# Kernel tuning notes

Measured on AMD Instinct MI355X. Metric: run time of the kernel, lower is better.

Reference implementation:

```python
import jax, jax.numpy as jnp
import numpy as np

B, S, D, H, DH, G, C, FF = 4, 4096, 768, 12, 64, 64, 256, 3072


def _ln(x, g, b):
    m = x.mean(-1, keepdims=True)
    v = ((x - m) ** 2).mean(-1, keepdims=True)
    return (x - m) * jax.lax.rsqrt(v + 1e-5) * g + b


def setup_inputs() -> dict:
    key = jax.random.key(0)
    ks = jax.random.split(key, 20)
    w = lambda k, shape: jax.random.normal(k, shape, jnp.float32) * 0.02
    inp = dict(
        cur_input=jax.random.normal(ks[0], (B, S, D), jnp.float32),
        prevLayerOutput=jax.random.normal(ks[1], (B, S, D), jnp.float32),
        classVector=jax.random.normal(ks[2], (B, C), jnp.float32),
        rand_idx=jax.random.randint(ks[3], (B, G), 0, S),
        # self-attention (rand+global) projections
        Wq=w(ks[4], (D, D)), bq=jnp.zeros(D), Wk=w(ks[5], (D, D)), bk=jnp.zeros(D),
        Wv=w(ks[6], (D, D)), bv=jnp.zeros(D), Wo=w(ks[7], (D, D)), bo=jnp.zeros(D),
        g1=jnp.ones(D), b1=jnp.zeros(D),
        # cross-attention over class vector (k/v feature dim is 1 after unsqueeze(-1))
        Wqc=w(ks[8], (D, D)), bqc=jnp.zeros(D), Wkc=w(ks[9], (1, D)), bkc=jnp.zeros(D),
        Wvc=w(ks[10], (1, D)), bvc=jnp.zeros(D), Woc=w(ks[11], (D, D)), boc=jnp.zeros(D),
        g2=jnp.ones(D), b2=jnp.zeros(D),
        # feed-forward
        W1=w(ks[12], (D, FF)), bf1=jnp.zeros(FF), W2=w(ks[13], (FF, D)), bf2=jnp.zeros(D),
        g3=jnp.ones(D), b3=jnp.zeros(D),
    )
    return inp


def reference(cur_input, prevLayerOutput, classVector, rand_idx,
              Wq, bq, Wk, bk, Wv, bv, Wo, bo, g1, b1,
              Wqc, bqc, Wkc, bkc, Wvc, bvc, Woc, boc, g2, b2,
              W1, bf1, W2, bf2, g3, b3):
    scale = np.float32(1.0 / np.sqrt(DH))
    # ---- masked multi-head self attention over global + random tokens ----
    q = (cur_input @ Wq + bq).reshape(B, S, H, DH)
    k = (prevLayerOutput @ Wk + bk).reshape(B, S, H, DH)
    v = (prevLayerOutput @ Wv + bv).reshape(B, S, H, DH)
    sel = jnp.concatenate([jnp.broadcast_to(jnp.arange(G), (B, G)), rand_idx], axis=1)  # [B,2G]
    idx = jnp.broadcast_to(sel[:, :, None, None], (B, 2 * G, H, DH))
    ksel = jnp.take_along_axis(k, idx, axis=1)  # [B,2G,H,DH]
    vsel = jnp.take_along_axis(v, idx, axis=1)
    scores = jnp.einsum('bshd,bkhd->bhsk', q, ksel) * scale  # [B,H,S,2G]
    mask = sel[:, None, None, :] <= jnp.arange(S)[None, None, :, None]  # causal wrt key position
    scores = jnp.where(mask, scores, jnp.float32(-1e9))
    attn = jax.nn.softmax(scores, axis=-1)
    o = jnp.einsum('bhsk,bkhd->bshd', attn, vsel).reshape(B, S, D) @ Wo + bo
    x1 = _ln(cur_input + o, g1, b1)
    # ---- cross attention over class vector (kv seq = C, kv feat = 1) ----
    cv = classVector[:, :, None]  # [B,C,1]
    qc = (x1 @ Wqc + bqc).reshape(B, S, H, DH)
    kc = (cv @ Wkc + bkc).reshape(B, C, H, DH)
    vc = (cv @ Wvc + bvc).reshape(B, C, H, DH)
    sc = jnp.einsum('bshd,bchd->bhsc', qc, kc) * scale
    ac = jax.nn.softmax(sc, axis=-1)
    oc = jnp.einsum('bhsc,bchd->bshd', ac, vc).reshape(B, S, D) @ Woc + boc
    x2 = _ln(x1 + oc, g2, b2)
    # ---- feed forward ----
    ff = jax.nn.relu(x2 @ W1 + bf1) @ W2 + bf2
    return _ln(x2 + ff, g3, b3)
```

## Files before the change

### kernel.cpp

```cpp
#include <hip/hip_runtime.h>
#include <hip/hip_bf16.h>

#define B_ 4
#define S_ 4096
#define D_ 768
#define H_ 12
#define DH_ 64
#define G_ 64
#define C_ 256
#define FF_ 3072

typedef __attribute__((ext_vector_type(8))) short bf16x8;
typedef __attribute__((ext_vector_type(4))) float f32x4;
typedef unsigned short u16;

__device__ __forceinline__ float bfu2f(u16 u) {
    return __uint_as_float((unsigned)u << 16);
}

__device__ __forceinline__ void gload16(const __hip_bfloat16* g, __hip_bfloat16* l) {
    __builtin_amdgcn_global_load_lds(
        (__attribute__((address_space(1))) void*)(void*)const_cast<__hip_bfloat16*>(g),
        (__attribute__((address_space(3))) void*)(void*)l,
        16, 0, 0);
}

__global__ __launch_bounds__(256) void gemm_mfma(
    const __hip_bfloat16* __restrict__ A, const __hip_bfloat16* __restrict__ Bt,
    const float* __restrict__ bias, float* __restrict__ Cf,
    __hip_bfloat16* __restrict__ Cb,
    int M, int N, int K, int lda, int ldbt, int flags)
{
    __shared__ __hip_bfloat16 As[2][128 * 32];
    __shared__ __hip_bfloat16 Bs[2][128 * 32];

    const int t = threadIdx.x;
    const int lane = t & 63;
    const int wave = t >> 6;
    const int wr = wave >> 1, wc = wave & 1;
    const int qd = lane >> 4, r = lane & 15;

    int lin = blockIdx.y * gridDim.x + blockIdx.x;
    int nwg = gridDim.x * gridDim.y;
    int cpx = nwg >> 3;
    int swz = (lin & 7) * cpx + (lin >> 3);
    int bm = (swz / gridDim.x) * 128;
    int bn = (swz % gridDim.x) * 128;

    const int srow = lane >> 2;
    const int scol = (lane & 3) * 8;
    const __hip_bfloat16* gA0 = A + (size_t)(bm + wave * 32 + srow) * lda + scol;
    const __hip_bfloat16* gA1 = gA0 + (size_t)16 * lda;
    const __hip_bfloat16* gB0 = Bt + (size_t)(bn + wave * 32 + srow) * ldbt + scol;
    const __hip_bfloat16* gB1 = gB0 + (size_t)16 * ldbt;

    f32x4 acc[4][4] = {};

    gload16(gA0, &As[0][wave * 1024]);
    gload16(gA1, &As[0][wave * 1024 + 512]);
    gload16(gB0, &Bs[0][wave * 1024]);
    gload16(gB1, &Bs[0][wave * 1024 + 512]);
    __syncthreads();

    int cur = 0;
    for (int k0 = 0; k0 < K; k0 += 32, cur ^= 1) {
        if (k0 + 32 < K) {
            int kn = k0 + 32, nb = cur ^ 1;
            gload16(gA0 + kn, &As[nb][wave * 1024]);
            gload16(gA1 + kn, &As[nb][wave * 1024 + 512]);
            gload16(gB0 + kn, &Bs[nb][wave * 1024]);
            gload16(gB1 + kn, &Bs[nb][wave * 1024 + 512]);
        }
        bf16x8 afr[4], bfr[4];
#pragma unroll
        for (int m = 0; m < 4; ++m)
            afr[m] = *(const bf16x8*)&As[cur][(wr * 64 + m * 16 + r) * 32 + qd * 8];
#pragma unroll
        for (int n = 0; n < 4; ++n)
            bfr[n] = *(const bf16x8*)&Bs[cur][(wc * 64 + n * 16 + r) * 32 + qd * 8];
#pragma unroll
        for (int m = 0; m < 4; ++m)
#pragma unroll
            for (int n = 0; n < 4; ++n)
                acc[m][n] = __builtin_amdgcn_mfma_f32_16x16x32_bf16(
                    afr[m], bfr[n], acc[m][n], 0, 0, 0);
        __syncthreads();
    }

#pragma unroll
    for (int m = 0; m < 4; ++m) {
        int row0 = bm + wr * 64 + m * 16 + qd * 4;
#pragma unroll
        for (int n = 0; n < 4; ++n) {
            int col = bn + wc * 64 + n * 16 + r;
            float bv = (flags & 1) ? bias[col] : 0.0f;
#pragma unroll
            for (int i = 0; i < 4; ++i) {
                float v = acc[m][n][i] + bv;
                if (flags & 2) v = fmaxf(v, 0.0f);
                size_t off = (size_t)(row0 + i) * N + col;
                if (flags & 4) v += Cf[off];
                if (flags & 8) Cb[off] = __float2bfloat16(v);
                else           Cf[off] = v;
            }
        }
    }
}

__global__ __launch_bounds__(256) void conv_bf16(const float* __restrict__ in,
                                                 __hip_bfloat16* __restrict__ out,
                                                 int n8)
{
    int i = blockIdx.x * 256 + threadIdx.x;
    if (i >= n8) return;
    const float4* p = (const float4*)(in + (size_t)i * 8);
    float4 v0 = p[0], v1 = p[1];
    __hip_bfloat16 o[8] = {
        __float2bfloat16(v0.x), __float2bfloat16(v0.y),
        __float2bfloat16(v0.z), __float2bfloat16(v0.w),
        __float2bfloat16(v1.x), __float2bfloat16(v1.y),
        __float2bfloat16(v1.z), __float2bfloat16(v1.w)};
    *(uint4*)(out + (size_t)i * 8) = *(const uint4*)o;
}

__global__ __launch_bounds__(256) void transp_all(
    const float* __restrict__ Wq, const float* __restrict__ Wo,
    const float* __restrict__ Wk, const float* __restrict__ Wv,
    const float* __restrict__ W1, const float* __restrict__ W2,
    __hip_bfloat16* __restrict__ Wqt, __hip_bfloat16* __restrict__ Wot,
    __hip_bfloat16* __restrict__ Wkt, __hip_bfloat16* __restrict__ Wvt,
    __hip_bfloat16* __restrict__ W1t, __hip_bfloat16* __restrict__ W2t)
{
    int tile = blockIdx.x;
    const float* W; __hip_bfloat16* Wt; int K, N;
    if (tile < 2304) {
        int w = tile / 576; tile -= w * 576;
        K = 768; N = 768;
        W  = (w == 0) ? Wq : (w == 1) ? Wo : (w == 2) ? Wk : Wv;
        Wt = (w == 0) ? Wqt : (w == 1) ? Wot : (w == 2) ? Wkt : Wvt;
    } else if (tile < 4608) { tile -= 2304; K = 768; N = 3072; W = W1; Wt = W1t; }
    else                    { tile -= 4608; K = 3072; N = 768; W = W2; Wt = W2t; }
    int ntx = N >> 5;
    int k0 = (tile / ntx) * 32, n0 = (tile % ntx) * 32;
    __shared__ float s[32][33];
    int tx = threadIdx.x & 31, ty = threadIdx.x >> 5;
#pragma unroll
    for (int i = 0; i < 4; ++i)
        s[ty + i * 8][tx] = W[(size_t)(k0 + ty + i * 8) * N + n0 + tx];
    __syncthreads();
#pragma unroll
    for (int i = 0; i < 4; ++i)
        Wt[(size_t)(n0 + ty + i * 8) * K + k0 + tx] =
            __float2bfloat16(s[tx][ty + i * 8]);
}

__global__ void gather_kernel(const float* __restrict__ prev,
                              const int* __restrict__ rand_idx,
                              __hip_bfloat16* __restrict__ Pselb,
                              int* __restrict__ sel)
{
    int j = blockIdx.x;
    int b = j >> 7, i = j & 127;
    int sv = (i < 64) ? i : rand_idx[b * G_ + (i - 64)];
    if (threadIdx.x == 0) sel[j] = sv;
    const float* src = prev + ((size_t)(b * S_ + sv)) * D_;
    __hip_bfloat16* dst = Pselb + (size_t)j * D_;
    for (int d = threadIdx.x; d < D_; d += blockDim.x)
        dst[d] = __float2bfloat16(src[d]);
}

__global__ __launch_bounds__(256) void attn3_kernel(
    const u16* __restrict__ qb, const u16* __restrict__ kb,
    const u16* __restrict__ vb, const int* __restrict__ sel,
    u16* __restrict__ out)
{
    const int bh = blockIdx.y;
    const int b = bh / H_, h = bh % H_;
    const int s0 = blockIdx.x * 256;
    const int t = threadIdx.x;
    const int w = t >> 6, lane = t & 63;
    const int r = lane & 15, qd = lane >> 4;

    __shared__ u16 Vt[64][136];
    __shared__ u16 Plds[4][32][136];
    __shared__ int ssel[128];

    {
        int key0 = t >> 4;
        int d0 = (t & 15) * 4;
        for (int kk = key0; kk < 128; kk += 16) {
            ushort4 v = *(const ushort4*)(vb + (size_t)(b * 128 + kk) * D_ + h * 64 + d0);
            Vt[d0 + 0][kk] = v.x; Vt[d0 + 1][kk] = v.y;
            Vt[d0 + 2][kk] = v.z; Vt[d0 + 3][kk] = v.w;
        }
        if (t < 128) ssel[t] = sel[b * 128 + t];
    }
    __syncthreads();

    int selv[8];
#pragma unroll
    for (int n = 0; n < 8; ++n) selv[n] = ssel[n * 16 + r];

    for (int pass = 0; pass < 2; ++pass) {
        const int sbase = s0 + w * 64 + pass * 32;
        f32x4 accs[2][8] = {};

#pragma unroll
        for (int ks = 0; ks < 2; ++ks) {
            bf16x8 af[2];
#pragma unroll
            for (int m = 0; m < 2; ++m)
                af[m] = *(const bf16x8*)(qb + (size_t)(b * S_ + sbase + m * 16 + r) * D_ + h * 64 + ks * 32 + qd * 8);
#pragma unroll
            for (int n = 0; n < 8; ++n) {
                bf16x8 bfv = *(const bf16x8*)(kb + (size_t)(b * 128 + n * 16 + r) * D_ + h * 64 + ks * 32 + qd * 8);
#pragma unroll
                for (int m = 0; m < 2; ++m)
                    accs[m][n] = __builtin_amdgcn_mfma_f32_16x16x32_bf16(
                        af[m], bfv, accs[m][n], 0, 0, 0);
            }
        }

#pragma unroll
        for (int m = 0; m < 2; ++m) {
#pragma unroll
            for (int i = 0; i < 4; ++i) {
                int srow = sbase + m * 16 + qd * 4 + i;
                float pm = -3e38f;
#pragma unroll
                for (int n = 0; n < 8; ++n) {
                    float sc = accs[m][n][i] * 0.125f;
                    if (selv[n] > srow) sc = -1e9f;
                    accs[m][n][i] = sc;
                    pm = fmaxf(pm, sc);
                }
#pragma unroll
                for (int off = 1; off < 16; off <<= 1)
                    pm = fmaxf(pm, __shfl_xor(pm, off, 64));
                float ps = 0.f;
#pragma unroll
                for (int n = 0; n < 8; ++n) {
                    float e = __expf(accs[m][n][i] - pm);
                    accs[m][n][i] = e;
                    ps += e;
                }
#pragma unroll
                for (int off = 1; off < 16; off <<= 1)
                    ps += __shfl_xor(ps, off, 64);
                float inv = 1.0f / ps;
#pragma unroll
                for (int n = 0; n < 8; ++n)
                    accs[m][n][i] *= inv;
            }
        }

#pragma unroll
        for (int m = 0; m < 2; ++m)
#pragma unroll
            for (int n = 0; n < 8; ++n)
#pragma unroll
                for (int i = 0; i < 4; ++i) {
                    __hip_bfloat16 pb = __float2bfloat16(accs[m][n][i]);
                    Plds[w][m * 16 + qd * 4 + i][n * 16 + r] = *(u16*)&pb;
                }

        f32x4 acco[2][4] = {};
#pragma unroll
        for (int ks = 0; ks < 4; ++ks) {
            bf16x8 pa[2];
#pragma unroll
            for (int m = 0; m < 2; ++m)
                pa[m] = *(const bf16x8*)&Plds[w][m * 16 + r][ks * 32 + qd * 8];
#pragma unroll
            for (int nd = 0; nd < 4; ++nd) {
                bf16x8 bv = *(const bf16x8*)&Vt[nd * 16 + r][ks * 32 + qd * 8];
#pragma unroll
                for (int m = 0; m < 2; ++m)
                    acco[m][nd] = __builtin_amdgcn_mfma_f32_16x16x32_bf16(
                        pa[m], bv, acco[m][nd], 0, 0, 0);
            }
        }

#pragma unroll
        for (int m = 0; m < 2; ++m)
#pragma unroll
            for (int nd = 0; nd < 4; ++nd)
#pragma unroll
                for (int i = 0; i < 4; ++i) {
                    __hip_bfloat16 ob = __float2bfloat16(acco[m][nd][i]);
                    out[(size_t)(b * S_ + sbase + m * 16 + qd * 4 + i) * D_ + h * 64 + nd * 16 + r] = *(u16*)&ob;
                }
    }
}

__global__ __launch_bounds__(192) void addln_bb(
    const u16* __restrict__ xa, const u16* __restrict__ xb,
    const float* __restrict__ g, const float* __restrict__ beta,
    float* __restrict__ out)
{
    const int row = blockIdx.x;
    const int t = threadIdx.x;
    const ushort4 a = ((const ushort4*)(xa + (size_t)row * D_))[t];
    const ushort4 b4 = ((const ushort4*)(xb + (size_t)row * D_))[t];
    float v[4] = {bfu2f(a.x) + bfu2f(b4.x), bfu2f(a.y) + bfu2f(b4.y),
                  bfu2f(a.z) + bfu2f(b4.z), bfu2f(a.w) + bfu2f(b4.w)};
    float sum = v[0] + v[1] + v[2] + v[3];
#pragma unroll
    for (int off = 1; off < 64; off <<= 1) sum += __shfl_xor(sum, off, 64);
    __shared__ float r1[3], r2[3];
    int wv = t >> 6, ln = t & 63;
    if (ln == 0) r1[wv] = sum;
    __syncthreads();
    float mean = (r1[0] + r1[1] + r1[2]) * (1.0f / 768.0f);
    float sq = 0.f;
#pragma unroll
    for (int i = 0; i < 4; ++i) { v[i] -= mean; sq += v[i] * v[i]; }
#pragma unroll
    for (int off = 1; off < 64; off <<= 1) sq += __shfl_xor(sq, off, 64);
    if (ln == 0) r2[wv] = sq;
    __syncthreads();
    float var = (r2[0] + r2[1] + r2[2]) * (1.0f / 768.0f);
    float rs = rsqrtf(var + 1e-5f);
    float4 gg = ((const float4*)g)[t];
    float4 bb = ((const float4*)beta)[t];
    float4 o;
    o.x = v[0] * rs * gg.x + bb.x;
    o.y = v[1] * rs * gg.y + bb.y;
    o.z = v[2] * rs * gg.z + bb.z;
    o.w = v[3] * rs * gg.w + bb.w;
    ((float4*)(out + (size_t)row * D_))[t] = o;
}

__global__ __launch_bounds__(256) void precompute_U(
    const float* __restrict__ Wqc, const float* __restrict__ Wkc,
    const float* __restrict__ bqc, float* __restrict__ Ut, float* __restrict__ ab)
{
    __shared__ __attribute__((aligned(16))) float wk[D_];
    for (int i = threadIdx.x; i < D_; i += 256) wk[i] = Wkc[i];
    __syncthreads();
    int idx = blockIdx.x * 256 + threadIdx.x;
    int h = idx / D_, d = idx - h * D_;
    const float4* row = (const float4*)(Wqc + (size_t)d * D_ + h * 64);
    const float4* wkv = (const float4*)(wk + h * 64);
    float a0 = 0.f, a1 = 0.f, a2 = 0.f, a3 = 0.f;
#pragma unroll
    for (int j = 0; j < 16; j += 4) {
        float4 r0 = row[j], r1 = row[j + 1], r2 = row[j + 2], r3 = row[j + 3];
        float4 c0 = wkv[j], c1 = wkv[j + 1], c2 = wkv[j + 2], c3 = wkv[j + 3];
        a0 += r0.x * c0.x + r0.y * c0.y + r0.z * c0.z + r0.w * c0.w;
        a1 += r1.x * c1.x + r1.y * c1.y + r1.z * c1.z + r1.w * c1.w;
        a2 += r2.x * c2.x + r2.y * c2.y + r2.z * c2.z + r2.w * c2.w;
        a3 += r3.x * c3.x + r3.y * c3.y + r3.z * c3.z + r3.w * c3.w;
    }
    Ut[idx] = (a0 + a1) + (a2 + a3);
    if (idx < H_) {
        const float4* bq4 = (const float4*)(bqc + idx * 64);
        const float4* wk4 = (const float4*)(wk + idx * 64);
        float s = 0.f;
#pragma unroll
        for (int j = 0; j < 16; ++j) {
            float4 bb = bq4[j], cc = wk4[j];
            s += bb.x * cc.x + bb.y * cc.y + bb.z * cc.z + bb.w * cc.w;
        }
        ab[idx] = s;
    }
}

__global__ __launch_bounds__(256) void precompute_mix(
    const float* __restrict__ Wvc, const float* __restrict__ Woc,
    float* __restrict__ Wmix)
{
    __shared__ float wv[D_];
    for (int i = threadIdx.x; i < D_; i += 256) wv[i] = Wvc[i];
    __syncthreads();
    int idx = blockIdx.x * 256 + threadIdx.x;
    int h = idx / D_, n = idx - h * D_;
    float acc[8] = {};
#pragma unroll
    for (int j = 0; j < 64; ++j)
        acc[j & 7] += wv[h * 64 + j] * Woc[(size_t)(h * 64 + j) * D_ + n];
    Wmix[idx] = ((acc[0] + acc[1]) + (acc[2] + acc[3]))
              + ((acc[4] + acc[5]) + (acc[6] + acc[7]));
}

__global__ __launch_bounds__(256) void precompute_bias2(
    const float* __restrict__ Woc, const float* __restrict__ bvc,
    const float* __restrict__ boc, float* __restrict__ bias2)
{
    int tx = threadIdx.x & 63, ty = threadIdx.x >> 6;
    int n = blockIdx.x * 64 + tx;
    int d0 = ty * 192;
    float a = 0.f;
#pragma unroll 8
    for (int d = 0; d < 192; ++d)
        a += bvc[d0 + d] * Woc[(size_t)(d0 + d) * D_ + n];
    __shared__ float red[4][64];
    red[ty][tx] = a;
    __syncthreads();
    if (ty == 0)
        bias2[n] = boc[n] + red[0][tx] + red[1][tx] + red[2][tx] + red[3][tx];
}

__global__ __launch_bounds__(256) void fused_mid(
    const float* __restrict__ cur, const u16* __restrict__ oprojb,
    const float* __restrict__ g1, const float* __restrict__ b1,
    const float* __restrict__ Ut, const float* __restrict__ ab,
    const float* __restrict__ cvec,
    const float* __restrict__ Wmix, const float* __restrict__ bias2,
    const float* __restrict__ g2, const float* __restrict__ b2,
    __hip_bfloat16* __restrict__ x2b)
{
    const int w = threadIdx.x >> 6, lane = threadIdx.x & 63;
    const int row0 = blockIdx.x * 8 + w * 2;
    const int b = blockIdx.x >> 9;

    __shared__ float4 cvs[64];
    __shared__ float xp[4][64][28];
    __shared__ float muls[4][24];

    if (threadIdx.x < 64)
        cvs[threadIdx.x] = ((const float4*)(cvec + b * C_))[threadIdx.x];

    float4 x1[2][3];
#pragma unroll
    for (int rr = 0; rr < 2; ++rr) {
        const float4* pa = (const float4*)(cur + (size_t)(row0 + rr) * D_);
        const ushort4* pb = (const ushort4*)(oprojb + (size_t)(row0 + rr) * D_);
        float s = 0.f;
#pragma unroll
        for (int i = 0; i < 3; ++i) {
            float4 a = pa[i * 64 + lane];
            ushort4 ou = pb[i * 64 + lane];
            float4 v;
            v.x = a.x + bfu2f(ou.x); v.y = a.y + bfu2f(ou.y);
            v.z = a.z + bfu2f(ou.z); v.w = a.w + bfu2f(ou.w);
            x1[rr][i] = v;
            s += v.x + v.y + v.z + v.w;
        }
#pragma unroll
        for (int off = 1; off < 64; off <<= 1) s += __shfl_xor(s, off, 64);
        float mean = s * (1.0f / 768.0f);
        float sq = 0.f;
#pragma unroll
        for (int i = 0; i < 3; ++i) {
            x1[rr][i].x -= mean; x1[rr][i].y -= mean;
            x1[rr][i].z -= mean; x1[rr][i].w -= mean;
            sq += x1[rr][i].x * x1[rr][i].x + x1[rr][i].y * x1[rr][i].y
                + x1[rr][i].z * x1[rr][i].z + x1[rr][i].w * x1[rr][i].w;
        }
#pragma unroll
        for (int off = 1; off < 64; off <<= 1) sq += __shfl_xor(sq, off, 64);
        float rs = rsqrtf(sq * (1.0f / 768.0f) + 1e-5f);
#pragma unroll
        for (int i = 0; i < 3; ++i) {
            float4 gg = ((const float4*)g1)[i * 64 + lane];
            float4 bb = ((const float4*)b1)[i * 64 + lane];
            x1[rr][i].x = x1[rr][i].x * rs * gg.x + bb.x;
            x1[rr][i].y = x1[rr][i].y * rs * gg.y + bb.y;
            x1[rr][i].z = x1[rr][i].z * rs * gg.z + bb.z;
            x1[rr][i].w = x1[rr][i].w * rs * gg.w + bb.w;
        }
    }

    float acc[24];
#pragma unroll
    for (int j = 0; j < 24; ++j) acc[j] = 0.f;
#pragma unroll
    for (int i = 0; i < 3; ++i) {
#pragma unroll
        for (int h = 0; h < 12; ++h) {
            float4 u = ((const float4*)(Ut + (size_t)h * D_))[i * 64 + lane];
#pragma unroll
            for (int rr = 0; rr < 2; ++rr)
                acc[rr * 12 + h] += x1[rr][i].x * u.x + x1[rr][i].y * u.y
                                  + x1[rr][i].z * u.z + x1[rr][i].w * u.w;
        }
    }
#pragma unroll
    for (int j4 = 0; j4 < 6; ++j4)
        *(float4*)&xp[w][lane][j4 * 4] = *(float4*)&acc[j4 * 4];
    __syncthreads();

    if (lane < 48) {
        int j = lane >> 1, half = lane & 1;
        float ssum = 0.f;
#pragma unroll
        for (int k = 0; k < 32; ++k) ssum += xp[w][half * 32 + k][j];
        ssum += __shfl_xor(ssum, 1, 64);
        float a = 0.125f * (ssum + ab[j % 12]);
        float z = 0.f, ms = 0.f;
#pragma unroll
        for (int it = 0; it < 32; ++it) {
            float4 c = cvs[half * 32 + it];
            float e0 = __expf(a * c.x), e1 = __expf(a * c.y),
                  e2 = __expf(a * c.z), e3 = __expf(a * c.w);
            z += e0 + e1 + e2 + e3;
            ms += e0 * c.x + e1 * c.y + e2 * c.z + e3 * c.w;
        }
        z += __shfl_xor(z, 1, 64);
        ms += __shfl_xor(ms, 1, 64);
        if (half == 0) muls[w][j] = ms / z;
    }
    __syncthreads();

    float4 t2[2][3];
#pragma unroll
    for (int i = 0; i < 3; ++i) {
        float4 bv = ((const float4*)bias2)[i * 64 + lane];
        float4 o0 = bv, o1 = bv;
#pragma unroll
        for (int h = 0; h < 12; ++h) {
            float4 wm = ((const float4*)(Wmix + (size_t)h * D_))[i * 64 + lane];
            float m0 = muls[w][h], m1 = muls[w][12 + h];
            o0.x += m0 * wm.x; o0.y += m0 * wm.y; o0.z += m0 * wm.z; o0.w += m0 * wm.w;
            o1.x += m1 * wm.x; o1.y += m1 * wm.y; o1.z += m1 * wm.z; o1.w += m1 * wm.w;
        }
        t2[0][i].x = x1[0][i].x + o0.x; t2[0][i].y = x1[0][i].y + o0.y;
        t2[0][i].z = x1[0][i].z + o0.z; t2[0][i].w = x1[0][i].w + o0.w;
        t2[1][i].x = x1[1][i].x + o1.x; t2[1][i].y = x1[1][i].y + o1.y;
        t2[1][i].z = x1[1][i].z + o1.z; t2[1][i].w = x1[1][i].w + o1.w;
    }

#pragma unroll
    for (int rr = 0; rr < 2; ++rr) {
        float s = 0.f;
#pragma unroll
        for (int i = 0; i < 3; ++i)
            s += t2[rr][i].x + t2[rr][i].y + t2[rr][i].z + t2[rr][i].w;
#pragma unroll
        for (int off = 1; off < 64; off <<= 1) s += __shfl_xor(s, off, 64);
        float mean = s * (1.0f / 768.0f);
        float sq = 0.f;
#pragma unroll
        for (int i = 0; i < 3; ++i) {
            t2[rr][i].x -= mean; t2[rr][i].y -= mean;
            t2[rr][i].z -= mean; t2[rr][i].w -= mean;
            sq += t2[rr][i].x * t2[rr][i].x + t2[rr][i].y * t2[rr][i].y
                + t2[rr][i].z * t2[rr][i].z + t2[rr][i].w * t2[rr][i].w;
        }
#pragma unroll
        for (int off = 1; off < 64; off <<= 1) sq += __shfl_xor(sq, off, 64);
        float rs = rsqrtf(sq * (1.0f / 768.0f) + 1e-5f);
        size_t base = (size_t)(row0 + rr) * D_;
#pragma unroll
        for (int i = 0; i < 3; ++i) {
            float4 gg = ((const float4*)g2)[i * 64 + lane];
            float4 bb = ((const float4*)b2)[i * 64 + lane];
            float vx = t2[rr][i].x * rs * gg.x + bb.x;
            float vy = t2[rr][i].y * rs * gg.y + bb.y;
            float vz = t2[rr][i].z * rs * gg.z + bb.z;
            float vw = t2[rr][i].w * rs * gg.w + bb.w;
            __hip_bfloat16 pk[4] = {
                __float2bfloat16(vx), __float2bfloat16(vy),
                __float2bfloat16(vz), __float2bfloat16(vw)};
            *(uint2*)(x2b + base + i * 256 + lane * 4) = *(const uint2*)pk;
        }
    }
}

extern "C" void kernel_launch(void* const* d_in, const int* in_sizes, int n_in,
                              void* d_out, int out_size, void* d_ws, size_t ws_size,
                              hipStream_t stream) {
    const float* cur   = (const float*)d_in[0];
    const float* prev  = (const float*)d_in[1];
    const float* cvec  = (const float*)d_in[2];
    const int*   ridx  = (const int*)d_in[3];
    const float* Wq  = (const float*)d_in[4];
    const float* bq  = (const float*)d_in[5];
    const float* Wk  = (const float*)d_in[6];
    const float* bk  = (const float*)d_in[7];
    const float* Wv  = (const float*)d_in[8];
    const float* bv  = (const float*)d_in[9];
    const float* Wo  = (const float*)d_in[10];
    const float* bo  = (const float*)d_in[11];
    const float* g1  = (const float*)d_in[12];
    const float* b1  = (const float*)d_in[13];
    const float* Wqc = (const float*)d_in[14];
    const float* bqc = (const float*)d_in[15];
    const float* Wkc = (const float*)d_in[16];
    const float* bkc = (const float*)d_in[17];  (void)bkc;
    const float* Wvc = (const float*)d_in[18];
    const float* bvc = (const float*)d_in[19];
    const float* Woc = (const float*)d_in[20];
    const float* boc = (const float*)d_in[21];
    const float* g2  = (const float*)d_in[22];
    const float* b2  = (const float*)d_in[23];
    const float* W1  = (const float*)d_in[24];
    const float* bf1 = (const float*)d_in[25];
    const float* W2  = (const float*)d_in[26];
    const float* bf2 = (const float*)d_in[27];
    const float* g3  = (const float*)d_in[28];
    const float* b3  = (const float*)d_in[29];
    float* outp = (float*)d_out;
    (void)ws_size; (void)in_sizes; (void)n_in; (void)out_size;

    const int M = B_ * S_;
    const size_t NBSD = (size_t)M * D_;
    const size_t NSEL = (size_t)B_ * 128 * D_;

    __hip_bfloat16* hidb  = (__hip_bfloat16*)d_ws;
    __hip_bfloat16* bf0   = hidb + (size_t)M * FF_;
    __hip_bfloat16* tmpb  = bf0 + NBSD;
    __hip_bfloat16* Pselb = tmpb + NBSD;
    __hip_bfloat16* kselb = Pselb + NSEL;
    __hip_bfloat16* vselb = kselb + NSEL;
    __hip_bfloat16* Wqt   = vselb + NSEL;
    __hip_bfloat16* Wot   = Wqt + (size_t)D_ * D_;
    __hip_bfloat16* Wkt   = Wot + (size_t)D_ * D_;
    __hip_bfloat16* Wvt   = Wkt + (size_t)D_ * D_;
    __hip_bfloat16* W1t   = Wvt + (size_t)D_ * D_;
    __hip_bfloat16* W2t   = W1t + (size_t)D_ * FF_;
    float* Ub    = (float*)(W2t + (size_t)FF_ * D_);
    float* abv   = Ub + (size_t)D_ * H_;
    float* Wmix  = abv + 16;
    float* bias2 = Wmix + (size_t)H_ * D_;
    int*   selb  = (int*)(bias2 + D_);

    gather_kernel<<<B_ * 128, 256, 0, stream>>>(prev, ridx, Pselb, selb);
    transp_all<<<6912, 256, 0, stream>>>(Wq, Wo, Wk, Wv, W1, W2,
                                         Wqt, Wot, Wkt, Wvt, W1t, W2t);
    conv_bf16<<<(int)(NBSD / 8 + 255) / 256, 256, 0, stream>>>(cur, bf0, (int)(NBSD / 8));
    precompute_U<<<36, 256, 0, stream>>>(Wqc, Wkc, bqc, Ub, abv);
    precompute_mix<<<36, 256, 0, stream>>>(Wvc, Woc, Wmix);
    precompute_bias2<<<12, 256, 0, stream>>>(Woc, bvc, boc, bias2);

    {
        dim3 g(D_ / 128, (B_ * 128) / 128);
        gemm_mfma<<<g, 256, 0, stream>>>(Pselb, Wkt, bk, nullptr, kselb,
                                         B_ * 128, D_, D_, D_, D_, 1 | 8);
        gemm_mfma<<<g, 256, 0, stream>>>(Pselb, Wvt, bv, nullptr, vselb,
                                         B_ * 128, D_, D_, D_, D_, 1 | 8);
    }

    gemm_mfma<<<dim3(D_ / 128, M / 128), 256, 0, stream>>>(
        bf0, Wqt, bq, nullptr, tmpb, M, D_, D_, D_, D_, 1 | 8);

    attn3_kernel<<<dim3(S_ / 256, B_ * H_), 256, 0, stream>>>(
        (const u16*)tmpb, (const u16*)kselb, (const u16*)vselb, selb, (u16*)bf0);

    gemm_mfma<<<dim3(D_ / 128, M / 128), 256, 0, stream>>>(
        bf0, Wot, bo, nullptr, tmpb, M, D_, D_, D_, D_, 1 | 8);

    fused_mid<<<M / 8, 256, 0, stream>>>(
        cur, (const u16*)tmpb, g1, b1, Ub, abv, cvec, Wmix, bias2, g2, b2, bf0);

    gemm_mfma<<<dim3(FF_ / 128, M / 128), 256, 0, stream>>>(
        bf0, W1t, bf1, nullptr, hidb, M, FF_, D_, D_, D_, 1 | 2 | 8);
    gemm_mfma<<<dim3(D_ / 128, M / 128), 256, 0, stream>>>(
        hidb, W2t, bf2, nullptr, tmpb, M, D_, FF_, FF_, FF_, 1 | 8);

    addln_bb<<<M, 192, 0, stream>>>((const u16*)bf0, (const u16*)tmpb, g3, b3, outp);
}
```

Measured before the change: 465.5 us.

## Add 256x256-tile 512-thread MFMA GEMM and use it for the big projections

```diff
diff --git a/kernel.cpp b/kernel.cpp
--- a/kernel.cpp
+++ b/kernel.cpp
@@ -23,6 +23,105 @@
         (__attribute__((address_space(1))) void*)(void*)const_cast<__hip_bfloat16*>(g),
         (__attribute__((address_space(3))) void*)(void*)l,
         16, 0, 0);
+}
+
+__global__ __launch_bounds__(512) void gemm256(
+    const u16* __restrict__ A, const u16* __restrict__ Bt,
+    const float* __restrict__ bias, u16* __restrict__ Cb,
+    int M, int N, int K, int flags)
+{
+    __shared__ __attribute__((aligned(16))) u16 As[2][256 * 64];
+    __shared__ __attribute__((aligned(16))) u16 Bs[2][256 * 64];
+
+    const int tid = threadIdx.x;
+    const int lane = tid & 63, w = tid >> 6;
+    const int wm = w >> 2, wn = w & 3;
+    const int r = lane & 15, qd = lane >> 4;
+
+    int lin = blockIdx.y * gridDim.x + blockIdx.x;
+    int nwg = gridDim.x * gridDim.y;
+    int cpx = nwg >> 3;
+    int swz = (lin & 7) * cpx + (lin >> 3);
+    int bm = (swz / gridDim.x) * 256;
+    int bn = (swz % gridDim.x) * 256;
+
+    const int srow = w * 8 + (lane >> 3);
+    const int scol = ((lane & 7) ^ (lane >> 3)) * 8;
+    const int sdst = w * 512;
+
+#define STAGE256(c, k0)                                                        \
+    {                                                                          \
+        _Pragma("unroll")                                                      \
+        for (int l = 0; l < 4; ++l)                                            \
+            gload16((const __hip_bfloat16*)(A + (size_t)(bm + srow + l * 64) * K + (k0) + scol), \
+                    (__hip_bfloat16*)&As[c][l * 4096 + sdst]);                 \
+        _Pragma("unroll")                                                      \
+        for (int l = 0; l < 4; ++l)                                            \
+            gload16((const __hip_bfloat16*)(Bt + (size_t)(bn + srow + l * 64) * K + (k0) + scol), \
+                    (__hip_bfloat16*)&Bs[c][l * 4096 + sdst]);                 \
+    }
+
+    f32x4 acc[8][4] = {};
+    const int NT = K >> 6;
+
+    STAGE256(0, 0)
+    STAGE256(1, 64)
+    asm volatile("s_waitcnt vmcnt(8)" ::: "memory");
+    __builtin_amdgcn_s_barrier();
+
+    for (int kt = 0; kt < NT; ++kt) {
+        const int c = kt & 1;
+        const u16* as = As[c];
+        const u16* bs = Bs[c];
+#pragma unroll
+        for (int kk = 0; kk < 2; ++kk) {
+            bf16x8 af[8], bfv[4];
+#pragma unroll
+            for (int m = 0; m < 8; ++m) {
+                int row = wm * 128 + m * 16 + r;
+                af[m] = *(const bf16x8*)&as[row * 64 + (((kk << 2) + qd) ^ (r & 7)) * 8];
+            }
+#pragma unroll
+            for (int n = 0; n < 4; ++n) {
+                int row = wn * 64 + n * 16 + r;
+                bfv[n] = *(const bf16x8*)&bs[row * 64 + (((kk << 2) + qd) ^ (r & 7)) * 8];
+            }
+            __builtin_amdgcn_s_setprio(1);
+#pragma unroll
+            for (int m = 0; m < 8; ++m)
+#pragma unroll
+                for (int n = 0; n < 4; ++n)
+                    acc[m][n] = __builtin_amdgcn_mfma_f32_16x16x32_bf16(
+                        af[m], bfv[n], acc[m][n], 0, 0, 0);
+            __builtin_amdgcn_s_setprio(0);
+        }
+        asm volatile("s_waitcnt lgkmcnt(0)" ::: "memory");
+        __builtin_amdgcn_s_barrier();
+        if (kt + 2 < NT) STAGE256(c, (kt + 2) << 6)
+        if (kt + 1 < NT) {
+            if (kt + 2 < NT) asm volatile("s_waitcnt vmcnt(8)" ::: "memory");
+            else             asm volatile("s_waitcnt vmcnt(0)" ::: "memory");
+            __builtin_amdgcn_s_barrier();
+        }
+    }
+
+#pragma unroll
+    for (int m = 0; m < 8; ++m) {
+        int row0 = bm + wm * 128 + m * 16 + qd * 4;
+#pragma unroll
+        for (int n = 0; n < 4; ++n) {
+            int col = bn + wn * 64 + n * 16 + r;
+            float bv = (flags & 1) ? bias[col] : 0.0f;
+#pragma unroll
+            for (int i = 0; i < 4; ++i) {
+                float v = acc[m][n][i] + bv;
+                if (flags & 2) v = fmaxf(v, 0.0f);
+                __hip_bfloat16 ob = __float2bfloat16(v);
+                Cb[(size_t)(row0 + i) * N + col] = *(u16*)&ob;
+            }
+        }
+    }
+#undef STAGE256
 }
 
 __global__ __launch_bounds__(256) void gemm_mfma(
@@ -632,22 +731,22 @@
                                          B_ * 128, D_, D_, D_, D_, 1 | 8);
     }
 
-    gemm_mfma<<<dim3(D_ / 128, M / 128), 256, 0, stream>>>(
-        bf0, Wqt, bq, nullptr, tmpb, M, D_, D_, D_, D_, 1 | 8);
+    gemm256<<<dim3(D_ / 256, M / 256), 512, 0, stream>>>(
+        (const u16*)bf0, (const u16*)Wqt, bq, (u16*)tmpb, M, D_, D_, 1);
 
     attn3_kernel<<<dim3(S_ / 256, B_ * H_), 256, 0, stream>>>(
         (const u16*)tmpb, (const u16*)kselb, (const u16*)vselb, selb, (u16*)bf0);
 
-    gemm_mfma<<<dim3(D_ / 128, M / 128), 256, 0, stream>>>(
-        bf0, Wot, bo, nullptr, tmpb, M, D_, D_, D_, D_, 1 | 8);
+    gemm256<<<dim3(D_ / 256, M / 256), 512, 0, stream>>>(
+        (const u16*)bf0, (const u16*)Wot, bo, (u16*)tmpb, M, D_, D_, 1);
 
     fused_mid<<<M / 8, 256, 0, stream>>>(
         cur, (const u16*)tmpb, g1, b1, Ub, abv, cvec, Wmix, bias2, g2, b2, bf0);
 
-    gemm_mfma<<<dim3(FF_ / 128, M / 128), 256, 0, stream>>>(
-        bf0, W1t, bf1, nullptr, hidb, M, FF_, D_, D_, D_, 1 | 2 | 8);
-    gemm_mfma<<<dim3(D_ / 128, M / 128), 256, 0, stream>>>(
-        hidb, W2t, bf2, nullptr, tmpb, M, D_, FF_, FF_, FF_, 1 | 8);
+    gemm256<<<dim3(FF_ / 256, M / 256), 512, 0, stream>>>(
+        (const u16*)bf0, (const u16*)W1t, bf1, (u16*)hidb, M, FF_, D_, 1 | 2);
+    gemm256<<<dim3(D_ / 256, M / 256), 512, 0, stream>>>(
+        (const u16*)hidb, (const u16*)W2t, bf2, (u16*)tmpb, M, D_, FF_, 1);
 
     addln_bb<<<M, 192, 0, stream>>>((const u16*)bf0, (const u16*)tmpb, g3, b3, outp);
 }
```

After: 450.6 us. 1.03x faster.

## Add 256x256-tile 8-wave pipelined MFMA GEMM for the large projections

Applied to the files above, without the earlier changes.

```diff
diff --git a/kernel.cpp b/kernel.cpp
--- a/kernel.cpp
+++ b/kernel.cpp
@@ -23,6 +23,149 @@
         (__attribute__((address_space(1))) void*)(void*)const_cast<__hip_bfloat16*>(g),
         (__attribute__((address_space(3))) void*)(void*)l,
         16, 0, 0);
+}
+
+__global__ __launch_bounds__(512, 2) void gemm256(
+    const u16* __restrict__ A, const u16* __restrict__ Bt,
+    const float* __restrict__ bias, u16* __restrict__ Cb,
+    int M, int N, int K, int flags)
+{
+    __shared__ __attribute__((aligned(16))) u16 Ah[2][2][128 * 64];
+    __shared__ __attribute__((aligned(16))) u16 Bh[2][2][128 * 64];
+
+    const int tid = threadIdx.x;
+    const int lane = tid & 63, w = tid >> 6;
+    const int wm = w >> 2, wn = w & 3;
+    const int r = lane & 15, qd = lane >> 4;
+
+    int lin = blockIdx.y * gridDim.x + blockIdx.x;
+    int nwg = gridDim.x * gridDim.y;
+    int cpx = nwg >> 3;
+    int swz = (lin & 7) * cpx + (lin >> 3);
+    int bm = (swz / gridDim.x) * 256;
+    int bn = (swz % gridDim.x) * 256;
+
+    const int srow = tid >> 3;
+    const int scol = ((tid & 7) ^ (srow & 7)) * 8;
+    const int sdst = tid * 8;
+
+#define STG_A(c, h, kt) { \
+    const u16* s_ = A + (size_t)(bm + (h) * 128 + srow) * K + ((kt) << 6) + scol; \
+    gload16((const __hip_bfloat16*)s_, (__hip_bfloat16*)&Ah[c][h][sdst]); \
+    gload16((const __hip_bfloat16*)(s_ + (size_t)64 * K), (__hip_bfloat16*)&Ah[c][h][sdst + 4096]); }
+#define STG_B(c, h, kt) { \
+    const u16* s_ = Bt + (size_t)(bn + (h) * 128 + srow) * K + ((kt) << 6) + scol; \
+    gload16((const __hip_bfloat16*)s_, (__hip_bfloat16*)&Bh[c][h][sdst]); \
+    gload16((const __hip_bfloat16*)(s_ + (size_t)64 * K), (__hip_bfloat16*)&Bh[c][h][sdst + 4096]); }
+
+#define GRAN(kk) (((((kk) << 2) + qd) ^ (r & 7)) * 8)
+#define READS_AF(c, mb) { \
+    _Pragma("unroll") for (int m = 0; m < 4; ++m) { \
+        const u16* p_ = &Ah[c][wm][((mb + m) * 16 + r) * 64]; \
+        af[m][0] = *(const bf16x8*)(p_ + GRAN(0)); \
+        af[m][1] = *(const bf16x8*)(p_ + GRAN(1)); } }
+#define READS_BF(dst, c, nb) { \
+    _Pragma("unroll") for (int n = 0; n < 2; ++n) { \
+        const u16* p_ = &Bh[c][wn >> 1][((wn & 1) * 64 + (nb + n) * 16 + r) * 64]; \
+        dst[n][0] = *(const bf16x8*)(p_ + GRAN(0)); \
+        dst[n][1] = *(const bf16x8*)(p_ + GRAN(1)); } }
+#define QMFMA(mb, nb, bfx) { \
+    __builtin_amdgcn_s_setprio(1); \
+    _Pragma("unroll") for (int kk = 0; kk < 2; ++kk) \
+    _Pragma("unroll") for (int m = 0; m < 4; ++m) \
+    _Pragma("unroll") for (int n = 0; n < 2; ++n) \
+        acc[mb + m][nb + n] = __builtin_amdgcn_mfma_f32_16x16x32_bf16( \
+            af[m][kk], bfx[n][kk], acc[mb + m][nb + n], 0, 0, 0); \
+    __builtin_amdgcn_s_setprio(0); }
+#define BAR() __builtin_amdgcn_s_barrier()
+#define LGKM0() asm volatile("s_waitcnt lgkmcnt(0)" ::: "memory")
+
+    f32x4 acc[8][4] = {};
+    const int NT = K >> 6;
+    const int J = NT >> 1;
+
+    STG_A(0, 0, 0) STG_A(0, 1, 0) STG_B(0, 0, 0) STG_B(0, 1, 0)
+    STG_B(1, 0, 1) STG_B(1, 1, 1)
+    asm volatile("s_waitcnt vmcnt(4)" ::: "memory");
+    BAR();
+
+    bf16x8 af[4][2], bf0[2][2], bf1[2][2];
+
+    for (int j = 0; j < J; ++j) {
+        const int to1 = 2 * j + 1;
+        const int te2 = 2 * j + 2;
+        const int to3 = 2 * j + 3;
+        const bool pf = (j < J - 1);
+
+        READS_AF(0, 0) READS_BF(bf0, 0, 0)
+        STG_A(1, 0, to1)
+        BAR(); LGKM0();
+        QMFMA(0, 0, bf0)
+        BAR();
+        READS_BF(bf1, 0, 2)
+        STG_A(1, 1, to1)
+        BAR(); LGKM0();
+        QMFMA(0, 2, bf1)
+        BAR();
+        READS_AF(0, 4)
+        if (pf) { STG_B(0, 0, te2) }
+        BAR(); LGKM0();
+        QMFMA(4, 2, bf1)
+        BAR();
+        if (pf) { STG_B(0, 1, te2) }
+        BAR();
+        QMFMA(4, 0, bf0)
+        if (pf) asm volatile("s_waitcnt vmcnt(4)" ::: "memory");
+        else    asm volatile("s_waitcnt vmcnt(0)" ::: "memory");
+        BAR();
+        READS_AF(1, 0) READS_BF(bf0, 1, 0)
+        if (pf) { STG_A(0, 0, te2) }
+        BAR(); LGKM0();
+        QMFMA(0, 0, bf0)
+        BAR();
+        READS_BF(bf1, 1, 2)
+        if (pf) { STG_A(0, 1, te2) }
+        BAR(); LGKM0();
+        QMFMA(0, 2, bf1)
+        BAR();
+        READS_AF(1, 4)
+        if (pf) { STG_B(1, 0, to3) }
+        BAR(); LGKM0();
+        QMFMA(4, 2, bf1)
+        BAR();
+        if (pf) { STG_B(1, 1, to3) }
+        BAR();
+        QMFMA(4, 0, bf0)
+        if (pf) {
+            asm volatile("s_waitcnt vmcnt(4)" ::: "memory");
+            BAR();
+        }
+    }
+
+#pragma unroll
+    for (int m = 0; m < 8; ++m) {
+        int row0 = bm + wm * 128 + m * 16 + qd * 4;
+#pragma unroll
+        for (int n = 0; n < 4; ++n) {
+            int col = bn + wn * 64 + n * 16 + r;
+            float bv = (flags & 1) ? bias[col] : 0.0f;
+#pragma unroll
+            for (int i = 0; i < 4; ++i) {
+                float v = acc[m][n][i] + bv;
+                if (flags & 2) v = fmaxf(v, 0.0f);
+                __hip_bfloat16 ob = __float2bfloat16(v);
+                Cb[(size_t)(row0 + i) * N + col] = *(u16*)&ob;
+            }
+        }
+    }
+#undef STG_A
+#undef STG_B
+#undef GRAN
+#undef READS_AF
+#undef READS_BF
+#undef QMFMA
+#undef BAR
+#undef LGKM0
 }
 
 __global__ __launch_bounds__(256) void gemm_mfma(
@@ -632,22 +775,22 @@
                                          B_ * 128, D_, D_, D_, D_, 1 | 8);
     }
 
-    gemm_mfma<<<dim3(D_ / 128, M / 128), 256, 0, stream>>>(
-        bf0, Wqt, bq, nullptr, tmpb, M, D_, D_, D_, D_, 1 | 8);
+    gemm256<<<dim3(D_ / 256, M / 256), 512, 0, stream>>>(
+        (const u16*)bf0, (const u16*)Wqt, bq, (u16*)tmpb, M, D_, D_, 1);
 
     attn3_kernel<<<dim3(S_ / 256, B_ * H_), 256, 0, stream>>>(
         (const u16*)tmpb, (const u16*)kselb, (const u16*)vselb, selb, (u16*)bf0);
 
-    gemm_mfma<<<dim3(D_ / 128, M / 128), 256, 0, stream>>>(
-        bf0, Wot, bo, nullptr, tmpb, M, D_, D_, D_, D_, 1 | 8);
+    gemm256<<<dim3(D_ / 256, M / 256), 512, 0, stream>>>(
+        (const u16*)bf0, (const u16*)Wot, bo, (u16*)tmpb, M, D_, D_, 1);
 
     fused_mid<<<M / 8, 256, 0, stream>>>(
         cur, (const u16*)tmpb, g1, b1, Ub, abv, cvec, Wmix, bias2, g2, b2, bf0);
 
-    gemm_mfma<<<dim3(FF_ / 128, M / 128), 256, 0, stream>>>(
-        bf0, W1t, bf1, nullptr, hidb, M, FF_, D_, D_, D_, 1 | 2 | 8);
-    gemm_mfma<<<dim3(D_ / 128, M / 128), 256, 0, stream>>>(
-        hidb, W2t, bf2, nullptr, tmpb, M, D_, FF_, FF_, FF_, 1 | 8);
+    gemm256<<<dim3(FF_ / 256, M / 256), 512, 0, stream>>>(
+        (const u16*)bf0, (const u16*)W1t, bf1, (u16*)hidb, M, FF_, D_, 1 | 2);
+    gemm256<<<dim3(D_ / 256, M / 256), 512, 0, stream>>>(
+        (const u16*)hidb, (const u16*)W2t, bf2, (u16*)tmpb, M, D_, FF_, 1);
 
     addln_bb<<<M, 192, 0, stream>>>((const u16*)bf0, (const u16*)tmpb, g3, b3, outp);
 }
```

Measured after the change: 438.3 us. 5.8% less time.

## Rewrite GEMM as 512-thread BK=64 swizzled-LDS kernel and read bf16 residual

Applied to the files above, without the earlier changes.

```diff
diff --git a/kernel.cpp b/kernel.cpp
--- a/kernel.cpp
+++ b/kernel.cpp
@@ -25,20 +25,18 @@
         16, 0, 0);
 }
 
-__global__ __launch_bounds__(256) void gemm_mfma(
-    const __hip_bfloat16* __restrict__ A, const __hip_bfloat16* __restrict__ Bt,
-    const float* __restrict__ bias, float* __restrict__ Cf,
-    __hip_bfloat16* __restrict__ Cb,
-    int M, int N, int K, int lda, int ldbt, int flags)
-{
-    __shared__ __hip_bfloat16 As[2][128 * 32];
-    __shared__ __hip_bfloat16 Bs[2][128 * 32];
-
-    const int t = threadIdx.x;
-    const int lane = t & 63;
-    const int wave = t >> 6;
-    const int wr = wave >> 1, wc = wave & 1;
-    const int qd = lane >> 4, r = lane & 15;
+__global__ __launch_bounds__(512, 4) void gemm128(
+    const u16* __restrict__ A, const u16* __restrict__ Bt,
+    const float* __restrict__ bias, u16* __restrict__ Cb,
+    int M, int N, int K, int flags)
+{
+    __shared__ __attribute__((aligned(16))) u16 As[2][128 * 64];
+    __shared__ __attribute__((aligned(16))) u16 Bs[2][128 * 64];
+
+    const int tid = threadIdx.x;
+    const int lane = tid & 63, w = tid >> 6;
+    const int wm = w >> 2, wn = w & 3;
+    const int r = lane & 15, qd = lane >> 4;
 
     int lin = blockIdx.y * gridDim.x + blockIdx.x;
     int nwg = gridDim.x * gridDim.y;
@@ -47,64 +45,76 @@
     int bm = (swz / gridDim.x) * 128;
     int bn = (swz % gridDim.x) * 128;
 
-    const int srow = lane >> 2;
-    const int scol = (lane & 3) * 8;
-    const __hip_bfloat16* gA0 = A + (size_t)(bm + wave * 32 + srow) * lda + scol;
-    const __hip_bfloat16* gA1 = gA0 + (size_t)16 * lda;
-    const __hip_bfloat16* gB0 = Bt + (size_t)(bn + wave * 32 + srow) * ldbt + scol;
-    const __hip_bfloat16* gB1 = gB0 + (size_t)16 * ldbt;
-
-    f32x4 acc[4][4] = {};
-
-    gload16(gA0, &As[0][wave * 1024]);
-    gload16(gA1, &As[0][wave * 1024 + 512]);
-    gload16(gB0, &Bs[0][wave * 1024]);
-    gload16(gB1, &Bs[0][wave * 1024 + 512]);
-    __syncthreads();
-
-    int cur = 0;
-    for (int k0 = 0; k0 < K; k0 += 32, cur ^= 1) {
-        if (k0 + 32 < K) {
-            int kn = k0 + 32, nb = cur ^ 1;
-            gload16(gA0 + kn, &As[nb][wave * 1024]);
-            gload16(gA1 + kn, &As[nb][wave * 1024 + 512]);
-            gload16(gB0 + kn, &Bs[nb][wave * 1024]);
-            gload16(gB1 + kn, &Bs[nb][wave * 1024 + 512]);
-        }
-        bf16x8 afr[4], bfr[4];
-#pragma unroll
-        for (int m = 0; m < 4; ++m)
-            afr[m] = *(const bf16x8*)&As[cur][(wr * 64 + m * 16 + r) * 32 + qd * 8];
-#pragma unroll
-        for (int n = 0; n < 4; ++n)
-            bfr[n] = *(const bf16x8*)&Bs[cur][(wc * 64 + n * 16 + r) * 32 + qd * 8];
-#pragma unroll
-        for (int m = 0; m < 4; ++m)
-#pragma unroll
-            for (int n = 0; n < 4; ++n)
-                acc[m][n] = __builtin_amdgcn_mfma_f32_16x16x32_bf16(
-                    afr[m], bfr[n], acc[m][n], 0, 0, 0);
-        __syncthreads();
+    const int srow = tid >> 3;
+    const int sg = ((tid & 7) ^ (srow & 7)) * 8;
+
+#define STG(c, kt) { \
+    const u16* a_ = A + (size_t)(bm + srow) * K + ((kt) << 6) + sg; \
+    gload16((const __hip_bfloat16*)a_, (__hip_bfloat16*)&As[c][tid * 8]); \
+    gload16((const __hip_bfloat16*)(a_ + (size_t)64 * K), (__hip_bfloat16*)&As[c][4096 + tid * 8]); \
+    const u16* b_ = Bt + (size_t)(bn + srow) * K + ((kt) << 6) + sg; \
+    gload16((const __hip_bfloat16*)b_, (__hip_bfloat16*)&Bs[c][tid * 8]); \
+    gload16((const __hip_bfloat16*)(b_ + (size_t)64 * K), (__hip_bfloat16*)&Bs[c][4096 + tid * 8]); }
+
+#define GR(kk) (((((kk) << 2) + qd) ^ (r & 7)) * 8)
+
+    f32x4 acc[4][2] = {};
+    const int NT = K >> 6;
+
+    STG(0, 0)
+    STG(1, 1)
+    asm volatile("s_waitcnt vmcnt(4)" ::: "memory");
+    __builtin_amdgcn_s_barrier();
+
+    for (int kt = 0; kt < NT; ++kt) {
+        const int c = kt & 1;
+        const u16* as = As[c];
+        const u16* bs = Bs[c];
+#pragma unroll
+        for (int kk = 0; kk < 2; ++kk) {
+            bf16x8 af[4], bf[2];
+#pragma unroll
+            for (int m = 0; m < 4; ++m)
+                af[m] = *(const bf16x8*)&as[(wm * 64 + m * 16 + r) * 64 + GR(kk)];
+#pragma unroll
+            for (int n = 0; n < 2; ++n)
+                bf[n] = *(const bf16x8*)&bs[(wn * 32 + n * 16 + r) * 64 + GR(kk)];
+            __builtin_amdgcn_s_setprio(1);
+#pragma unroll
+            for (int m = 0; m < 4; ++m)
+#pragma unroll
+                for (int n = 0; n < 2; ++n)
+                    acc[m][n] = __builtin_amdgcn_mfma_f32_16x16x32_bf16(
+                        af[m], bf[n], acc[m][n], 0, 0, 0);
+            __builtin_amdgcn_s_setprio(0);
+        }
+        __builtin_amdgcn_s_barrier();
+        if (kt + 2 < NT) STG(c, kt + 2)
+        if (kt + 1 < NT) {
+            if (kt + 2 < NT) asm volatile("s_waitcnt vmcnt(4)" ::: "memory");
+            else             asm volatile("s_waitcnt vmcnt(0)" ::: "memory");
+            __builtin_amdgcn_s_barrier();
+        }
     }
 
 #pragma unroll
     for (int m = 0; m < 4; ++m) {
-        int row0 = bm + wr * 64 + m * 16 + qd * 4;
-#pragma unroll
-        for (int n = 0; n < 4; ++n) {
-            int col = bn + wc * 64 + n * 16 + r;
+        int row0 = bm + wm * 64 + m * 16 + qd * 4;
+#pragma unroll
+        for (int n = 0; n < 2; ++n) {
+            int col = bn + wn * 32 + n * 16 + r;
             float bv = (flags & 1) ? bias[col] : 0.0f;
 #pragma unroll
             for (int i = 0; i < 4; ++i) {
                 float v = acc[m][n][i] + bv;
                 if (flags & 2) v = fmaxf(v, 0.0f);
-                size_t off = (size_t)(row0 + i) * N + col;
-                if (flags & 4) v += Cf[off];
-                if (flags & 8) Cb[off] = __float2bfloat16(v);
-                else           Cf[off] = v;
+                __hip_bfloat16 ob = __float2bfloat16(v);
+                Cb[(size_t)(row0 + i) * N + col] = *(u16*)&ob;
             }
         }
     }
+#undef STG
+#undef GR
 }
 
 __global__ __launch_bounds__(256) void conv_bf16(const float* __restrict__ in,
@@ -402,7 +412,7 @@
 }
 
 __global__ __launch_bounds__(256) void fused_mid(
-    const float* __restrict__ cur, const u16* __restrict__ oprojb,
+    const u16* __restrict__ curb, const u16* __restrict__ oprojb,
     const float* __restrict__ g1, const float* __restrict__ b1,
     const float* __restrict__ Ut, const float* __restrict__ ab,
     const float* __restrict__ cvec,
@@ -424,16 +434,16 @@
     float4 x1[2][3];
 #pragma unroll
     for (int rr = 0; rr < 2; ++rr) {
-        const float4* pa = (const float4*)(cur + (size_t)(row0 + rr) * D_);
+        const ushort4* pa = (const ushort4*)(curb + (size_t)(row0 + rr) * D_);
         const ushort4* pb = (const ushort4*)(oprojb + (size_t)(row0 + rr) * D_);
         float s = 0.f;
 #pragma unroll
         for (int i = 0; i < 3; ++i) {
-            float4 a = pa[i * 64 + lane];
+            ushort4 au = pa[i * 64 + lane];
             ushort4 ou = pb[i * 64 + lane];
             float4 v;
-            v.x = a.x + bfu2f(ou.x); v.y = a.y + bfu2f(ou.y);
-            v.z = a.z + bfu2f(ou.z); v.w = a.w + bfu2f(ou.w);
+            v.x = bfu2f(au.x) + bfu2f(ou.x); v.y = bfu2f(au.y) + bfu2f(ou.y);
+            v.z = bfu2f(au.z) + bfu2f(ou.z); v.w = bfu2f(au.w) + bfu2f(ou.w);
             x1[rr][i] = v;
             s += v.x + v.y + v.z + v.w;
         }
@@ -626,28 +636,29 @@
 
     {
         dim3 g(D_ / 128, (B_ * 128) / 128);
-        gemm_mfma<<<g, 256, 0, stream>>>(Pselb, Wkt, bk, nullptr, kselb,
-                                         B_ * 128, D_, D_, D_, D_, 1 | 8);
-        gemm_mfma<<<g, 256, 0, stream>>>(Pselb, Wvt, bv, nullptr, vselb,
-                                         B_ * 128, D_, D_, D_, D_, 1 | 8);
-    }
-
-    gemm_mfma<<<dim3(D_ / 128, M / 128), 256, 0, stream>>>(
-        bf0, Wqt, bq, nullptr, tmpb, M, D_, D_, D_, D_, 1 | 8);
+        gemm128<<<g, 512, 0, stream>>>((const u16*)Pselb, (const u16*)Wkt, bk,
+                                       (u16*)kselb, B_ * 128, D_, D_, 1);
+        gemm128<<<g, 512, 0, stream>>>((const u16*)Pselb, (const u16*)Wvt, bv,
+                                       (u16*)vselb, B_ * 128, D_, D_, 1);
+    }
+
+    gemm128<<<dim3(D_ / 128, M / 128), 512, 0, stream>>>(
+        (const u16*)bf0, (const u16*)Wqt, bq, (u16*)tmpb, M, D_, D_, 1);
 
     attn3_kernel<<<dim3(S_ / 256, B_ * H_), 256, 0, stream>>>(
-        (const u16*)tmpb, (const u16*)kselb, (const u16*)vselb, selb, (u16*)bf0);
-
-    gemm_mfma<<<dim3(D_ / 128, M / 128), 256, 0, stream>>>(
-        bf0, Wot, bo, nullptr, tmpb, M, D_, D_, D_, D_, 1 | 8);
+        (const u16*)tmpb, (const u16*)kselb, (const u16*)vselb, selb, (u16*)hidb);
+
+    gemm128<<<dim3(D_ / 128, M / 128), 512, 0, stream>>>(
+        (const u16*)hidb, (const u16*)Wot, bo, (u16*)tmpb, M, D_, D_, 1);
 
     fused_mid<<<M / 8, 256, 0, stream>>>(
-        cur, (const u16*)tmpb, g1, b1, Ub, abv, cvec, Wmix, bias2, g2, b2, bf0);
-
-    gemm_mfma<<<dim3(FF_ / 128, M / 128), 256, 0, stream>>>(
-        bf0, W1t, bf1, nullptr, hidb, M, FF_, D_, D_, D_, 1 | 2 | 8);
-    gemm_mfma<<<dim3(D_ / 128, M / 128), 256, 0, stream>>>(
-        hidb, W2t, bf2, nullptr, tmpb, M, D_, FF_, FF_, FF_, 1 | 8);
+        (const u16*)bf0, (const u16*)tmpb, g1, b1, Ub, abv, cvec, Wmix, bias2,
+        g2, b2, bf0);
+
+    gemm128<<<dim3(FF_ / 128, M / 128), 512, 0, stream>>>(
+        (const u16*)bf0, (const u16*)W1t, bf1, (u16*)hidb, M, FF_, D_, 1 | 2);
+    gemm128<<<dim3(D_ / 128, M / 128), 512, 0, stream>>>(
+        (const u16*)hidb, (const u16*)W2t, bf2, (u16*)tmpb, M, D_, FF_, 1);
 
     addln_bb<<<M, 192, 0, stream>>>((const u16*)bf0, (const u16*)tmpb, g3, b3, outp);
 }
```

Result: faster. 428.6 us (-7.9%).
